# Kernel tuning notes

Hardware: AMD Instinct MI355X
Metric: run time of the kernel (lower is better)

The kernel has to match this reference:

```python
import jax, jax.numpy as jnp
import numpy as np

N = 4096

def setup_inputs() -> dict:
    key = jax.random.key(0)
    kA, kB = jax.random.split(key)
    A = jnp.tril(jax.random.normal(kA, (N, N), dtype=jnp.float32))
    B = jnp.tril(jax.random.normal(kB, (N, N), dtype=jnp.float32))
    return {"A": A, "B": B}

def reference(A, B):
    # Product of two lower-triangular matrices; result is lower-triangular.
    # tril applied to the dense matmul reproduces the intended math exactly
    # (and zeroes any numerical noise in the structural-zero upper triangle).
    return jnp.tril(jnp.matmul(A, B))
```

## Files before the change

### kernel.cpp

```cpp
#include <hip/hip_runtime.h>
#include <stdint.h>

#define NN 4096
#define NB2 16
#define BK 64

#define NUNITS 260
#define ZBASE 260
#define TGRID 380
#define NSPLIT 78
#define NWSLOTS 202

#define PGRID_W 8192
#define PGRID_A 8504

typedef __bf16 bf16x8 __attribute__((ext_vector_type(8)));
typedef float f32x4 __attribute__((ext_vector_type(4)));
typedef unsigned short ushort8 __attribute__((ext_vector_type(8)));

__device__ __forceinline__ unsigned short f2bf(float x) {
    union { float f; unsigned int u; } v; v.f = x;
    unsigned int u = v.u;
    u += 0x7fffu + ((u >> 16) & 1u);
    return (unsigned short)(u >> 16);
}

#define GLOAD16(g, l) __builtin_amdgcn_global_load_lds( \
    (const __attribute__((address_space(1))) unsigned int*)(g), \
    (__attribute__((address_space(3))) unsigned int*)(l), 16, 0, 0)

__device__ __forceinline__ void split_decode(int z, int& bi, int& bj, int& nu, int& u0) {
    int d = 15, acc = 0;
    for (;;) {
        nu = (d + 4) >> 2;
        int cnt = NB2 - d;
        if (z < cnt) { bj = z; bi = z + d; u0 = acc + z * nu; return; }
        z -= cnt; acc += cnt * nu; --d;
    }
}

__global__ __launch_bounds__(256) void prep(const float* __restrict__ A,
                                            const float* __restrict__ B,
                                            unsigned short* __restrict__ Ab,
                                            unsigned short* __restrict__ Bt,
                                            float* __restrict__ C) {
    __shared__ float tile[64][65];
    int bid = blockIdx.x;
    int tid = threadIdx.x;

    if (bid < 4096) {
        int i = bid;
        int nslots = ((i >> 8) + 1) * 32;
        const float4* src = reinterpret_cast<const float4*>(A + (size_t)i * NN);
        unsigned short* dst = Ab + (size_t)i * NN;
        for (int p = tid; p < nslots; p += 256) {
            float4 x0 = src[p * 2], x1 = src[p * 2 + 1];
            ushort8 o;
            o[0] = f2bf(x0.x); o[1] = f2bf(x0.y); o[2] = f2bf(x0.z); o[3] = f2bf(x0.w);
            o[4] = f2bf(x1.x); o[5] = f2bf(x1.y); o[6] = f2bf(x1.z); o[7] = f2bf(x1.w);
            *reinterpret_cast<ushort8*>(dst + p * 8) = o;
        }
        return;
    }
    if (bid < 8192) {
        int s = bid - 4096;
        int n64 = s >> 6, k64 = s & 63;
        if (k64 < (n64 & ~3)) return;
        int n0 = n64 * 64, k0 = k64 * 64;
        int tx = tid & 63, ty = tid >> 6;
#pragma unroll
        for (int r = 0; r < 16; ++r) {
            int k = ty + r * 4;
            tile[k][tx] = B[(size_t)(k0 + k) * NN + n0 + tx];
        }
        __syncthreads();
#pragma unroll
        for (int r = 0; r < 16; ++r) {
            int n = ty + r * 4;
            Bt[(size_t)(n0 + n) * NN + k0 + tx] = f2bf(tile[tx][n]);
        }
        return;
    }
    {
        int z = bid - 8192;
        int bi, bj, nu, u0; split_decode(z >> 2, bi, bj, nu, u0);
        int part = z & 3;
        float4 zf = make_float4(0.f, 0.f, 0.f, 0.f);
        float4* cp = reinterpret_cast<float4*>(C + (size_t)(bi * 256 + part * 64) * NN + (size_t)bj * 256);
#pragma unroll
        for (int i2 = 0; i2 < 16; ++i2) {
            int slot = tid + i2 * 256;
            int row = slot >> 6, c4 = slot & 63;
            cp[(size_t)row * (NN / 4) + c4] = zf;
        }
    }
}

__global__ __launch_bounds__(512, 1) void trimm(const unsigned short* __restrict__ Ab,
                                                const unsigned short* __restrict__ Bt,
                                                float* __restrict__ C,
                                                float* __restrict__ W,
                                                int useW) {
    int bid = blockIdx.x;
    int tid = threadIdx.x;
    int lane = tid & 63;
    int w = tid >> 6;

    if (bid >= ZBASE) {
        int r = bid - ZBASE, bi = 0;
        while (r >= NB2 - 1 - bi) { r -= NB2 - 1 - bi; ++bi; }
        int bj = bi + 1 + r;
        float4 z = make_float4(0.f, 0.f, 0.f, 0.f);
        float4* cp = reinterpret_cast<float4*>(C + (size_t)bi * 256 * NN + (size_t)bj * 256);
#pragma unroll
        for (int i2 = 0; i2 < 32; ++i2) {
            int slot = tid + i2 * 512;
            int row = slot >> 6, c4 = slot & 63;
            cp[(size_t)row * (NN / 4) + c4] = z;
        }
        return;
    }

    int bi, bj, k_lo, nt;
    bool atom;
    {
        int r = bid, d = 15, nu;
        for (;;) {
            nu = (d + 4) >> 2;
            int cnt = (NB2 - d) * nu;
            if (r < cnt) break;
            r -= cnt; --d;
        }
        int t = r / nu, part = r - t * nu;
        bj = t; bi = t + d;
        atom = (nu > 1);
        int ntk = 4 * (d + 1);
        int ntb = ntk / nu, rem = ntk % nu;
        nt = ntb + (part < rem ? 1 : 0);
        int skip = part * ntb + (part < rem ? part : rem);
        k_lo = bj * 256 + skip * BK;
    }

    __shared__ unsigned short As[4][128 * 64];
    __shared__ unsigned short Bs[4][128 * 64];

    int qwr = w >> 2;
    int qwc = w & 3;
    int fr = lane & 15;
    int c0 = (((lane >> 4) ^ (lane & 7)) * 8);
    int c1 = ((((lane >> 4) | 4) ^ (lane & 7)) * 8);

    int srow = tid >> 3;
    int schunk = ((tid & 7) ^ (srow & 7)) * 8;
    const unsigned short* gA = Ab + (size_t)(bi * 256 + srow) * NN + schunk;
    const unsigned short* gB = Bt + (size_t)(bj * 256 + srow) * NN + schunk;

    f32x4 acc[4][4][2];
#pragma unroll
    for (int q = 0; q < 4; ++q)
#pragma unroll
        for (int m = 0; m < 4; ++m)
#pragma unroll
            for (int n = 0; n < 2; ++n)
                acc[q][m][n] = (f32x4){0.f, 0.f, 0.f, 0.f};

    bf16x8 a0[4], a1[4], bh0c0[2], bh0c1[2], bh1c0[2], bh1c1[2];

#define STG(XS, gX, h, slot, kk) do { \
        unsigned short* d_ = &XS[slot][0] + tid * 8; \
        GLOAD16(gX + (size_t)(h) * 128 * NN + (kk), d_); \
        GLOAD16(gX + (size_t)((h) * 128 + 64) * NN + (kk), d_ + 4096); \
    } while (0)

#define LDAH(slot, AV0, AV1) do { \
        _Pragma("unroll") for (int m_ = 0; m_ < 4; ++m_) { \
            int r_ = (qwr * 64 + m_ * 16 + fr) * 64; \
            AV0[m_] = *reinterpret_cast<const bf16x8*>(&As[slot][r_ + c0]); \
            AV1[m_] = *reinterpret_cast<const bf16x8*>(&As[slot][r_ + c1]); \
        } \
    } while (0)

#define LDBH(slot, B0V, B1V) do { \
        _Pragma("unroll") for (int n_ = 0; n_ < 2; ++n_) { \
            int r_ = (qwc * 32 + n_ * 16 + fr) * 64; \
            B0V[n_] = *reinterpret_cast<const bf16x8*>(&Bs[slot][r_ + c0]); \
            B1V[n_] = *reinterpret_cast<const bf16x8*>(&Bs[slot][r_ + c1]); \
        } \
    } while (0)

#define MFMAQ(Q, AV0, AV1, B0V, B1V) do { \
        _Pragma("unroll") for (int m_ = 0; m_ < 4; ++m_) \
        _Pragma("unroll") for (int n_ = 0; n_ < 2; ++n_) { \
            acc[Q][m_][n_] = __builtin_amdgcn_mfma_f32_16x16x32_bf16(AV0[m_], B0V[n_], acc[Q][m_][n_], 0, 0, 0); \
            acc[Q][m_][n_] = __builtin_amdgcn_mfma_f32_16x16x32_bf16(AV1[m_], B1V[n_], acc[Q][m_][n_], 0, 0, 0); \
        } \
    } while (0)

#define BAR __builtin_amdgcn_s_barrier()

    STG(As, gA, 0, 0, k_lo);
    STG(Bs, gB, 0, 0, k_lo);
    STG(Bs, gB, 1, 1, k_lo);
    STG(As, gA, 1, 1, k_lo);

    for (int t = 0; t < nt; ++t) {
        int p = (t & 1) << 1;
        int np = p ^ 2;
        int kkn = (t + 1 < nt) ? (k_lo + (t + 1) * BK) : k_lo;

        asm volatile("s_waitcnt vmcnt(2)" ::: "memory");
        BAR;
        LDAH(p, a0, a1);
        LDBH(p, bh0c0, bh0c1);
        LDBH(p | 1, bh1c0, bh1c1);
        __builtin_amdgcn_s_setprio(1);
        MFMAQ(0, a0, a1, bh0c0, bh0c1);
        MFMAQ(1, a0, a1, bh1c0, bh1c1);
        __builtin_amdgcn_s_setprio(0);
        STG(As, gA, 0, np, kkn);
        STG(Bs, gB, 0, np, kkn);

        asm volatile("s_waitcnt vmcnt(4)" ::: "memory");
        BAR;
        LDAH(p | 1, a0, a1);
        __builtin_amdgcn_s_setprio(1);
        MFMAQ(2, a0, a1, bh1c0, bh1c1);
        MFMAQ(3, a0, a1, bh0c0, bh0c1);
        __builtin_amdgcn_s_setprio(0);
        STG(Bs, gB, 1, np | 1, kkn);
        STG(As, gA, 1, np | 1, kkn);
    }
    asm volatile("s_waitcnt vmcnt(0)" ::: "memory");
#undef STG
#undef LDAH
#undef LDBH
#undef MFMAQ
#undef BAR

    int r4 = (lane >> 4) * 4;
    if (atom && useW) {
        float* wb = W + (size_t)bid * 65536;
#pragma unroll
        for (int q = 0; q < 4; ++q) {
            int mh = q >> 1, nh = ((q + 1) >> 1) & 1;
#pragma unroll
            for (int m = 0; m < 4; ++m)
#pragma unroll
                for (int n = 0; n < 2; ++n) {
                    int row = mh * 128 + qwr * 64 + m * 16 + r4;
                    int col = nh * 128 + qwc * 32 + n * 16 + fr;
                    float* wp = wb + (size_t)row * 256 + col;
#pragma unroll
                    for (int r2 = 0; r2 < 4; ++r2)
                        wp[r2 * 256] = acc[q][m][n][r2];
                }
        }
    } else if (atom) {
#pragma unroll
        for (int q = 0; q < 4; ++q) {
            int mh = q >> 1, nh = ((q + 1) >> 1) & 1;
#pragma unroll
            for (int m = 0; m < 4; ++m)
#pragma unroll
                for (int n = 0; n < 2; ++n) {
                    int row = bi * 256 + mh * 128 + qwr * 64 + m * 16 + r4;
                    int col = bj * 256 + nh * 128 + qwc * 32 + n * 16 + fr;
                    float* cp = C + (size_t)row * NN + col;
#pragma unroll
                    for (int r2 = 0; r2 < 4; ++r2)
                        atomicAdd(&cp[(size_t)r2 * NN], acc[q][m][n][r2]);
                }
        }
    } else {
#pragma unroll
        for (int q = 0; q < 4; ++q) {
            int mh = q >> 1, nh = ((q + 1) >> 1) & 1;
#pragma unroll
            for (int m = 0; m < 4; ++m)
#pragma unroll
                for (int n = 0; n < 2; ++n) {
                    int row = bi * 256 + mh * 128 + qwr * 64 + m * 16 + r4;
                    int col = bj * 256 + nh * 128 + qwc * 32 + n * 16 + fr;
                    float* cp = C + (size_t)row * NN + col;
#pragma unroll
                    for (int r2 = 0; r2 < 4; ++r2)
                        cp[(size_t)r2 * NN] = acc[q][m][n][r2];
                }
        }
    }
}

__global__ __launch_bounds__(256) void merge(const float* __restrict__ W,
                                             float* __restrict__ C) {
    int blk = blockIdx.x;
    int z = blk >> 3;
    int sub = blk & 7;
    int tid = threadIdx.x;
    int bi, bj, nu, u0; split_decode(z, bi, bj, nu, u0);
    const float4* w0 = reinterpret_cast<const float4*>(W + (size_t)u0 * 65536) + sub * 2048;
#pragma unroll 2
    for (int it = 0; it < 8; ++it) {
        int s = tid + it * 256;
        int row = s >> 6, c4 = s & 63;
        float4 a = w0[s];
        for (int p = 1; p < nu; ++p) {
            float4 b = w0[(size_t)p * 16384 + s];
            a.x += b.x; a.y += b.y; a.z += b.z; a.w += b.w;
        }
        float4* cp = reinterpret_cast<float4*>(C) +
                     (size_t)(bi * 256 + sub * 32 + row) * (NN / 4) + bj * 64 + c4;
        *cp = a;
    }
}

extern "C" void kernel_launch(void* const* d_in, const int* in_sizes, int n_in,
                              void* d_out, int out_size, void* d_ws, size_t ws_size,
                              hipStream_t stream) {
    const float* A = (const float*)d_in[0];
    const float* B = (const float*)d_in[1];
    float* C = (float*)d_out;
    unsigned short* Ab = (unsigned short*)d_ws;
    unsigned short* Bt = Ab + (size_t)NN * NN;
    const size_t base = (size_t)2 * NN * NN * sizeof(unsigned short);
    const size_t wbytes = (size_t)NWSLOTS * 65536 * sizeof(float);
    const int useW = (ws_size >= base + wbytes) ? 1 : 0;
    float* W = (float*)((char*)d_ws + base);

    prep<<<useW ? PGRID_W : PGRID_A, 256, 0, stream>>>(A, B, Ab, Bt, C);
    trimm<<<TGRID, 512, 0, stream>>>(Ab, Bt, C, W, useW);
    if (useW) merge<<<NSPLIT * 8, 256, 0, stream>>>(W, C);
}
```

Measured before the change: 76.75 us.

## Restructure GEMM main loop into four barrier-gated MFMA clusters with interleaved loads

Splits each K-iteration into four phases, each issuing LDS fragment reads and one global-to-LDS stage, then a vmcnt wait, a barrier, an lgkmcnt gate and a prioritized MFMA cluster followed by another barrier. The aim is to interleave memory traffic with MFMA work at finer grain, in a ping-pong style schedule across waves. It adds more barriers per iteration, which can cost synchronization overhead. Reordering stage writes against reads of the same buffers also risks LDS hazards if the wait counts are off.

```diff
diff --git a/kernel.cpp b/kernel.cpp
--- a/kernel.cpp
+++ b/kernel.cpp
@@ -164,7 +164,7 @@
             for (int n = 0; n < 2; ++n)
                 acc[q][m][n] = (f32x4){0.f, 0.f, 0.f, 0.f};
 
-    bf16x8 a0[4], a1[4], bh0c0[2], bh0c1[2], bh1c0[2], bh1c1[2];
+    bf16x8 a0[4], a1[4], b0c0[2], b0c1[2], b1c0[2], b1c1[2];
 
 #define STG(XS, gX, h, slot, kk) do { \
         unsigned short* d_ = &XS[slot][0] + tid * 8; \
@@ -196,46 +196,64 @@
         } \
     } while (0)
 
+#define VMC4 asm volatile("s_waitcnt vmcnt(4)" ::: "memory")
 #define BAR __builtin_amdgcn_s_barrier()
+#define CLUSTER_GATE do { \
+        asm volatile("s_waitcnt lgkmcnt(0)" ::: "memory"); \
+        __builtin_amdgcn_sched_barrier(0); \
+    } while (0)
+#define PRIO1 __builtin_amdgcn_s_setprio(1)
+#define PRIO0 __builtin_amdgcn_s_setprio(0)
 
     STG(As, gA, 0, 0, k_lo);
     STG(Bs, gB, 0, 0, k_lo);
     STG(Bs, gB, 1, 1, k_lo);
     STG(As, gA, 1, 1, k_lo);
+    VMC4; BAR;
 
     for (int t = 0; t < nt; ++t) {
         int p = (t & 1) << 1;
         int np = p ^ 2;
         int kkn = (t + 1 < nt) ? (k_lo + (t + 1) * BK) : k_lo;
 
-        asm volatile("s_waitcnt vmcnt(2)" ::: "memory");
-        BAR;
         LDAH(p, a0, a1);
-        LDBH(p, bh0c0, bh0c1);
-        LDBH(p | 1, bh1c0, bh1c1);
-        __builtin_amdgcn_s_setprio(1);
-        MFMAQ(0, a0, a1, bh0c0, bh0c1);
-        MFMAQ(1, a0, a1, bh1c0, bh1c1);
-        __builtin_amdgcn_s_setprio(0);
+        LDBH(p, b0c0, b0c1);
         STG(As, gA, 0, np, kkn);
+        VMC4; BAR;
+        CLUSTER_GATE;
+        PRIO1; MFMAQ(0, a0, a1, b0c0, b0c1); PRIO0;
+        BAR;
+
+        LDBH(p | 1, b1c0, b1c1);
         STG(Bs, gB, 0, np, kkn);
-
-        asm volatile("s_waitcnt vmcnt(4)" ::: "memory");
-        BAR;
+        VMC4; BAR;
+        CLUSTER_GATE;
+        PRIO1; MFMAQ(1, a0, a1, b1c0, b1c1); PRIO0;
+        BAR;
+
         LDAH(p | 1, a0, a1);
-        __builtin_amdgcn_s_setprio(1);
-        MFMAQ(2, a0, a1, bh1c0, bh1c1);
-        MFMAQ(3, a0, a1, bh0c0, bh0c1);
-        __builtin_amdgcn_s_setprio(0);
         STG(Bs, gB, 1, np | 1, kkn);
+        BAR;
+        CLUSTER_GATE;
+        PRIO1; MFMAQ(2, a0, a1, b1c0, b1c1); PRIO0;
+        BAR;
+
         STG(As, gA, 1, np | 1, kkn);
+        VMC4; BAR;
+        CLUSTER_GATE;
+        PRIO1; MFMAQ(3, a0, a1, b0c0, b0c1); PRIO0;
+        BAR;
     }
     asm volatile("s_waitcnt vmcnt(0)" ::: "memory");
 #undef STG
 #undef LDAH
 #undef LDBH
 #undef MFMAQ
+#undef VMC4
 #undef BAR
+#undef CLUSTER_GATE
+#undef PRIO1
+#undef PRIO0
 
     int r4 = (lane >> 4) * 4;
     if (atom && useW) {
```

After: 77.74 us. Within noise of the previous version (+1.3%).

## Remap warps to contiguous 128x64 subtiles with single-barrier interleaved pipeline

Applied to the files above, without the earlier changes.

Each warp now owns one contiguous 128x64 region of the 256x256 output tile instead of four scattered quadrant pieces, so each warp reads only one A half and one B half from shared memory. The main loop changes from two barrier phases with explicit vmcnt waits to one __syncthreads per iteration. LDS reads are split by k-half, and global staging is interleaved between MFMA groups. The aim is to cut LDS read traffic and barrier stalls. The risks are more register pressure from larger per-warp fragments and possibly less precise load/compute overlap without the explicit waitcnt.

```diff
diff --git a/kernel.cpp b/kernel.cpp
--- a/kernel.cpp
+++ b/kernel.cpp
@@ -144,8 +144,10 @@
     __shared__ unsigned short As[4][128 * 64];
     __shared__ unsigned short Bs[4][128 * 64];
 
-    int qwr = w >> 2;
-    int qwc = w & 3;
+    int wr = w >> 2;
+    int wc = w & 3;
+    int hb = wc >> 1;
+    int colb = (wc & 1) * 64;
     int fr = lane & 15;
     int c0 = (((lane >> 4) ^ (lane & 7)) * 8);
     int c1 = ((((lane >> 4) | 4) ^ (lane & 7)) * 8);
@@ -155,16 +157,14 @@
     const unsigned short* gA = Ab + (size_t)(bi * 256 + srow) * NN + schunk;
     const unsigned short* gB = Bt + (size_t)(bj * 256 + srow) * NN + schunk;
 
-    f32x4 acc[4][4][2];
-#pragma unroll
-    for (int q = 0; q < 4; ++q)
-#pragma unroll
-        for (int m = 0; m < 4; ++m)
-#pragma unroll
-            for (int n = 0; n < 2; ++n)
-                acc[q][m][n] = (f32x4){0.f, 0.f, 0.f, 0.f};
-
-    bf16x8 a0[4], a1[4], bh0c0[2], bh0c1[2], bh1c0[2], bh1c1[2];
+    f32x4 acc[8][4];
+#pragma unroll
+    for (int m = 0; m < 8; ++m)
+#pragma unroll
+        for (int n = 0; n < 4; ++n)
+            acc[m][n] = (f32x4){0.f, 0.f, 0.f, 0.f};
+
+    bf16x8 aX[4], aY[4], bv0[4], bv1[4];
 
 #define STG(XS, gX, h, slot, kk) do { \
         unsigned short* d_ = &XS[slot][0] + tid * 8; \
@@ -172,31 +172,28 @@
         GLOAD16(gX + (size_t)((h) * 128 + 64) * NN + (kk), d_ + 4096); \
     } while (0)
 
-#define LDAH(slot, AV0, AV1) do { \
+#define RDA(Ap, G, CC, AV) do { \
         _Pragma("unroll") for (int m_ = 0; m_ < 4; ++m_) { \
-            int r_ = (qwr * 64 + m_ * 16 + fr) * 64; \
-            AV0[m_] = *reinterpret_cast<const bf16x8*>(&As[slot][r_ + c0]); \
-            AV1[m_] = *reinterpret_cast<const bf16x8*>(&As[slot][r_ + c1]); \
+            int r_ = (((G) * 4 + m_) * 16 + fr) * 64; \
+            AV[m_] = *reinterpret_cast<const bf16x8*>(&Ap[r_ + (CC)]); \
         } \
     } while (0)
 
-#define LDBH(slot, B0V, B1V) do { \
-        _Pragma("unroll") for (int n_ = 0; n_ < 2; ++n_) { \
-            int r_ = (qwc * 32 + n_ * 16 + fr) * 64; \
-            B0V[n_] = *reinterpret_cast<const bf16x8*>(&Bs[slot][r_ + c0]); \
-            B1V[n_] = *reinterpret_cast<const bf16x8*>(&Bs[slot][r_ + c1]); \
+#define RDB(Bp, CC, BV) do { \
+        _Pragma("unroll") for (int n_ = 0; n_ < 4; ++n_) { \
+            int r_ = (colb + n_ * 16 + fr) * 64; \
+            BV[n_] = *reinterpret_cast<const bf16x8*>(&Bp[r_ + (CC)]); \
         } \
     } while (0)
 
-#define MFMAQ(Q, AV0, AV1, B0V, B1V) do { \
+#define MFMA16(AV, BV, MB) do { \
         _Pragma("unroll") for (int m_ = 0; m_ < 4; ++m_) \
-        _Pragma("unroll") for (int n_ = 0; n_ < 2; ++n_) { \
-            acc[Q][m_][n_] = __builtin_amdgcn_mfma_f32_16x16x32_bf16(AV0[m_], B0V[n_], acc[Q][m_][n_], 0, 0, 0); \
-            acc[Q][m_][n_] = __builtin_amdgcn_mfma_f32_16x16x32_bf16(AV1[m_], B1V[n_], acc[Q][m_][n_], 0, 0, 0); \
-        } \
+        _Pragma("unroll") for (int n_ = 0; n_ < 4; ++n_) \
+            acc[(MB) + m_][n_] = __builtin_amdgcn_mfma_f32_16x16x32_bf16(AV[m_], BV[n_], acc[(MB) + m_][n_], 0, 0, 0); \
     } while (0)
 
-#define BAR __builtin_amdgcn_s_barrier()
+#define PRIO1 __builtin_amdgcn_s_setprio(1)
+#define PRIO0 __builtin_amdgcn_s_setprio(0)
 
     STG(As, gA, 0, 0, k_lo);
     STG(Bs, gB, 0, 0, k_lo);
@@ -204,89 +201,74 @@
     STG(As, gA, 1, 1, k_lo);
 
     for (int t = 0; t < nt; ++t) {
-        int p = (t & 1) << 1;
-        int np = p ^ 2;
+        __syncthreads();
+
+        const unsigned short* Ac = &As[(2 * t + wr) & 3][0];
+        const unsigned short* Bc = &Bs[(2 * t + hb) & 3][0];
+        int np0 = (2 * t + 2) & 3, np1 = (2 * t + 3) & 3;
         int kkn = (t + 1 < nt) ? (k_lo + (t + 1) * BK) : k_lo;
 
-        asm volatile("s_waitcnt vmcnt(2)" ::: "memory");
-        BAR;
-        LDAH(p, a0, a1);
-        LDBH(p, bh0c0, bh0c1);
-        LDBH(p | 1, bh1c0, bh1c1);
-        __builtin_amdgcn_s_setprio(1);
-        MFMAQ(0, a0, a1, bh0c0, bh0c1);
-        MFMAQ(1, a0, a1, bh1c0, bh1c1);
-        __builtin_amdgcn_s_setprio(0);
-        STG(As, gA, 0, np, kkn);
-        STG(Bs, gB, 0, np, kkn);
-
-        asm volatile("s_waitcnt vmcnt(4)" ::: "memory");
-        BAR;
-        LDAH(p | 1, a0, a1);
-        __builtin_amdgcn_s_setprio(1);
-        MFMAQ(2, a0, a1, bh1c0, bh1c1);
-        MFMAQ(3, a0, a1, bh0c0, bh0c1);
-        __builtin_amdgcn_s_setprio(0);
-        STG(Bs, gB, 1, np | 1, kkn);
-        STG(As, gA, 1, np | 1, kkn);
+        RDA(Ac, 0, c0, aX);
+        RDB(Bc, c0, bv0);
+        RDA(Ac, 1, c0, aY);
+        STG(As, gA, 0, np0, kkn);
+        STG(Bs, gB, 0, np0, kkn);
+        PRIO1; MFMA16(aX, bv0, 0); PRIO0;
+        RDA(Ac, 0, c1, aX);
+        RDB(Bc, c1, bv1);
+        STG(Bs, gB, 1, np1, kkn);
+        STG(As, gA, 1, np1, kkn);
+        PRIO1; MFMA16(aY, bv0, 4); PRIO0;
+        RDA(Ac, 1, c1, aY);
+        PRIO1; MFMA16(aX, bv1, 0); PRIO0;
+        PRIO1; MFMA16(aY, bv1, 4); PRIO0;
     }
     asm volatile("s_waitcnt vmcnt(0)" ::: "memory");
 #undef STG
-#undef LDAH
-#undef LDBH
-#undef MFMAQ
-#undef BAR
+#undef RDA
+#undef RDB
+#undef MFMA16
+#undef PRIO1
+#undef PRIO0
 
     int r4 = (lane >> 4) * 4;
     if (atom && useW) {
         float* wb = W + (size_t)bid * 65536;
 #pragma unroll
-        for (int q = 0; q < 4; ++q) {
-            int mh = q >> 1, nh = ((q + 1) >> 1) & 1;
-#pragma unroll
-            for (int m = 0; m < 4; ++m)
-#pragma unroll
-                for (int n = 0; n < 2; ++n) {
-                    int row = mh * 128 + qwr * 64 + m * 16 + r4;
-                    int col = nh * 128 + qwc * 32 + n * 16 + fr;
-                    float* wp = wb + (size_t)row * 256 + col;
-#pragma unroll
-                    for (int r2 = 0; r2 < 4; ++r2)
-                        wp[r2 * 256] = acc[q][m][n][r2];
-                }
-        }
+        for (int m = 0; m < 8; ++m)
+#pragma unroll
+            for (int n = 0; n < 4; ++n) {
+                int row = wr * 128 + m * 16 + r4;
+                int col = wc * 64 + n * 16 + fr;
+                float* wp = wb + (size_t)row * 256 + col;
+#pragma unroll
+                for (int r2 = 0; r2 < 4; ++r2)
+                    wp[(size_t)r2 * 256] = acc[m][n][r2];
+            }
     } else if (atom) {
 #pragma unroll
-        for (int q = 0; q < 4; ++q) {
-            int mh = q >> 1, nh = ((q + 1) >> 1) & 1;
-#pragma unroll
-            for (int m = 0; m < 4; ++m)
-#pragma unroll
-                for (int n = 0; n < 2; ++n) {
-                    int row = bi * 256 + mh * 128 + qwr * 64 + m * 16 + r4;
-                    int col = bj * 256 + nh * 128 + qwc * 32 + n * 16 + fr;
-                    float* cp = C + (size_t)row * NN + col;
-#pragma unroll
-                    for (int r2 = 0; r2 < 4; ++r2)
-                        atomicAdd(&cp[(size_t)r2 * NN], acc[q][m][n][r2]);
-                }
-        }
+        for (int m = 0; m < 8; ++m)
+#pragma unroll
+            for (int n = 0; n < 4; ++n) {
+                int row = bi * 256 + wr * 128 + m * 16 + r4;
+                int col = bj * 256 + wc * 64 + n * 16 + fr;
+                float* cp = C + (size_t)row * NN + col;
+#pragma unroll
+                for (int r2 = 0; r2 < 4; ++r2)
+                    atomicAdd(&cp[(size_t)r2 * NN], acc[m][n][r2]);
+            }
     } else {
 #pragma unroll
-        for (int q = 0; q < 4; ++q) {
-            int mh = q >> 1, nh = ((q + 1) >> 1) & 1;
-#pragma unroll
-            for (int m = 0; m < 4; ++m)
-#pragma unroll
-                for (int n = 0; n < 2; ++n) {
-                    int row = bi * 256 + mh * 128 + qwr * 64 + m * 16 + r4;
-                    int col = bj * 256 + nh * 128 + qwc * 32 + n * 16 + fr;
-                    float* cp = C + (size_t)row * NN + col;
-#pragma unroll
-                    for (int r2 = 0; r2 < 4; ++r2)
-                        cp[(size_t)r2 * NN] = acc[q][m][n][r2];
-                }
-        }
+        for (int m = 0; m < 8; ++m)
+#pragma unroll
+            for (int n = 0; n < 4; ++n) {
+                int row = bi * 256 + wr * 128 + m * 16 + r4;
+                int col = bj * 256 + wc * 64 + n * 16 + fr;
+                float* cp = C + (size_t)row * NN + col;
+#pragma unroll
+                for (int r2 = 0; r2 < 4; ++r2)
+                    cp[(size_t)r2 * NN] = acc[m][n][r2];
+            }
     }
 }
 
```

Result: slower. 79.47 us (+3.5%).
